# Kernel optimization log

Hardware: AMD Instinct MI355X
Metric: run time of the kernel (lower is better)

Reference implementation:

```python
import jax, jax.numpy as jnp
import numpy as np
from jax import lax

BOOST_STRENGTH = 0.5
WEIGHT_DENSITY = 0.05


def setup_inputs() -> dict:
    key = jax.random.key(0)
    k1, k2, k3, k4, k5 = jax.random.split(key, 5)
    batch, d_in, d_out = 16384, 512, 4096
    x = jax.random.normal(k1, (batch, d_in), dtype=jnp.float32)
    W = jax.random.normal(k2, (d_out, d_in), dtype=jnp.float32) * 0.05
    b = jax.random.normal(k3, (d_out,), dtype=jnp.float32) * 0.01
    w_mask = (jax.random.uniform(k4, (d_out, d_in)) < WEIGHT_DENSITY).astype(jnp.float32)
    # duty cycle buffer in [0, 0.1]
    duty_cycle = jax.random.uniform(k5, (d_out,), dtype=jnp.float32) * 0.1
    k = 205  # round(0.05 * 4096)
    return {"x": x, "W": W, "b": b, "w_mask": w_mask,
            "duty_cycle": duty_cycle, "k": k}


def reference(x, W, b, w_mask, duty_cycle, k):
    # SparseWeights: masked dense linear
    y = x @ (W * w_mask).T + b                      # [B, n]
    n = y.shape[-1]
    target_density = k / n
    # KWinners boosting: exp of duty-cycle deficit
    boost = jnp.exp(BOOST_STRENGTH * (target_density - duty_cycle))  # [n]
    boosted = y * boost                              # [B, n]
    # top-k threshold per row on boosted values
    thresh = lax.top_k(boosted, k)[0][..., -1:]      # [B, 1]
    # mask: keep ORIGINAL activations at winner positions
    return jnp.where(boosted >= thresh, y, 0.0)
```

## Files before the change

kernel.cpp:

```cpp
#include <hip/hip_runtime.h>
#include <stdint.h>
#include <math.h>


#define BATCH 16384
#define K_DIM 512
#define N_DIM 4096
#define MAXE 64
#define ROWS_A 64

typedef float f32x4 __attribute__((ext_vector_type(4)));
typedef unsigned int u32;

__global__ void boost_kernel(const float* __restrict__ duty,
                             const int* __restrict__ kptr,
                             float* __restrict__ boost) {
  const int j = blockIdx.x * blockDim.x + threadIdx.x;
  if (j < N_DIM) {
    const float td = (float)((double)kptr[0] / (double)N_DIM);
    const float arg = 0.5f * (td - duty[j]);
    boost[j] = (float)exp((double)arg);
  }
}

__global__ __launch_bounds__(256) void compress_kernel(
    const float* __restrict__ W, const float* __restrict__ mask,
    unsigned short* __restrict__ cIdx, float* __restrict__ cVal,
    int* __restrict__ cnt) {
  const int j = blockIdx.x * 4 + (threadIdx.x >> 6);
  const int lane = threadIdx.x & 63;
  if (j >= N_DIM) return;
  const float* mr = mask + (size_t)j * K_DIM;
  const float* wr = W + (size_t)j * K_DIM;
  int base = 0;
#pragma unroll
  for (int c = 0; c < K_DIM / 64; ++c) {
    const int k = c * 64 + lane;
    const bool act = (mr[k] != 0.0f);
    const unsigned long long bal = __ballot(act);
    const int pos = __popcll(bal & ((1ull << lane) - 1ull));
    if (act && base + pos < MAXE) {
      cIdx[(size_t)j * MAXE + base + pos] = (unsigned short)k;
      cVal[(size_t)j * MAXE + base + pos] = wr[k];
    }
    base += (int)__popcll(bal);
  }
  if (lane == 0) cnt[j] = base < MAXE ? base : MAXE;
}

__global__ __launch_bounds__(256) void cmax_kernel(
    const int* __restrict__ cnt, int* __restrict__ cm4) {
  const int i = blockIdx.x * 256 + threadIdx.x;
  const int4 c = *(const int4*)(cnt + i * 4);
  int m = c.x > c.y ? c.x : c.y;
  m = c.z > m ? c.z : m;
  m = c.w > m ? c.w : m;
  cm4[i] = (m + 3) & ~3;
}

__global__ __launch_bounds__(256) void fillA_kernel(
    const unsigned short* __restrict__ cIdx, const float* __restrict__ cVal,
    const int* __restrict__ cnt, uint2* __restrict__ pairsA) {
  const int idx = blockIdx.x * 256 + threadIdx.x;
  const int j = idx >> 6;
  const int e = idx & 63;
  uint2 pr;
  if (e < cnt[j]) {
    pr.x = (u32)cIdx[(size_t)j * MAXE + e] << 16;
    pr.y = __float_as_uint(cVal[(size_t)j * MAXE + e]);
  } else {
    pr.x = 0u; pr.y = 0u;
  }
  pairsA[idx] = pr;
}

__global__ __launch_bounds__(256) void transpose_kernel(
    const float* __restrict__ x, float* __restrict__ xTg) {
  __shared__ float t[64][65];
  const int lane = threadIdx.x & 63;
  const int quad = threadIdx.x >> 6;
  const int kb = (blockIdx.x & 7) * 64;
  const int rb = (blockIdx.x >> 3) * 64;
#pragma unroll
  for (int i = 0; i < 16; ++i) {
    const int r = quad * 16 + i;
    t[lane][r] = x[(size_t)(rb + r) * K_DIM + kb + lane];
  }
  __syncthreads();
#pragma unroll
  for (int i = 0; i < 16; ++i) {
    const int kq = quad * 16 + i;
    xTg[(size_t)(kb + kq) * BATCH + rb + lane] = t[kq][lane];
  }
}

__global__ __launch_bounds__(1024, 4) void fold_kernel(
    const float* __restrict__ xTg, const uint2* __restrict__ pairsA,
    const int* __restrict__ cm4, float* __restrict__ y) {
  const int tid = threadIdx.x;
  const int lane = tid & 63;
  const int wave = __builtin_amdgcn_readfirstlane(tid >> 6);
  const int row0 = blockIdx.x * ROWS_A;
  const char* xb = (const char*)(xTg + row0);
  const u32 vb = (u32)(lane << 2);

  const int jbase = wave * 256;

#pragma unroll 1
  for (int g = 0; g < 8; ++g) {
    float acc[32];
#pragma unroll
    for (int q = 0; q < 32; ++q) acc[q] = 0.0f;

#pragma unroll
    for (int sub = 0; sub < 8; ++sub) {
      const int j0 = jbase + g * 32 + sub * 4;
      const int cmax = cm4[j0 >> 2];
      const uint2* p0 = pairsA + (size_t)(j0 + 0) * MAXE;
      const uint2* p1 = pairsA + (size_t)(j0 + 1) * MAXE;
      const uint2* p2 = pairsA + (size_t)(j0 + 2) * MAXE;
      const uint2* p3 = pairsA + (size_t)(j0 + 3) * MAXE;
      float a0 = 0.0f, a1 = 0.0f, a2 = 0.0f, a3 = 0.0f;
#pragma unroll 1
      for (int e = 0; e < cmax; e += 4) {
#pragma unroll
        for (int q = 0; q < 4; ++q) {
          const uint2 e0 = p0[e + q];
          const uint2 e1 = p1[e + q];
          const uint2 e2 = p2[e + q];
          const uint2 e3 = p3[e + q];
          const float x0 = *(const float*)(xb + (e0.x + vb));
          const float x1 = *(const float*)(xb + (e1.x + vb));
          const float x2 = *(const float*)(xb + (e2.x + vb));
          const float x3 = *(const float*)(xb + (e3.x + vb));
          a0 = fmaf(__uint_as_float(e0.y), x0, a0);
          a1 = fmaf(__uint_as_float(e1.y), x1, a1);
          a2 = fmaf(__uint_as_float(e2.y), x2, a2);
          a3 = fmaf(__uint_as_float(e3.y), x3, a3);
        }
      }
      acc[sub * 4 + 0] = a0;
      acc[sub * 4 + 1] = a1;
      acc[sub * 4 + 2] = a2;
      acc[sub * 4 + 3] = a3;
    }

    float* yp = y + (size_t)(row0 + lane) * N_DIM + jbase + g * 32;
#pragma unroll
    for (int q = 0; q < 8; ++q)
      *(f32x4*)(yp + q * 4) =
          (f32x4){acc[q * 4], acc[q * 4 + 1], acc[q * 4 + 2], acc[q * 4 + 3]};
  }
}

__global__ __launch_bounds__(256) void select_kernel(
    const float* __restrict__ bvec, const float* __restrict__ boost,
    const int* __restrict__ kptr, float* __restrict__ out) {
  const int lane = threadIdx.x & 63;
  const int row = blockIdx.x * 4 + (threadIdx.x >> 6);
  const u32 kk = (u32)kptr[0];
  float* orow = out + (size_t)row * N_DIM;

  u32 kv[64];
#pragma unroll
  for (int v = 0; v < 16; ++v) {
    const int j = v * 256 + lane * 4;
    const f32x4 a = *(const f32x4*)(orow + j);
    const f32x4 b = *(const f32x4*)(bvec + j);
    const f32x4 gv = *(const f32x4*)(boost + j);
#pragma unroll
    for (int q = 0; q < 4; ++q) {
      const float yy = a[q] + b[q];
      const u32 u = __float_as_uint(yy * gv[q]);
      kv[v * 4 + q] = (u & 0x80000000u) ? ~u : (u | 0x80000000u);
    }
  }

  u32 P = 0u;
#pragma unroll 1
  for (int bit = 31; bit >= 0; --bit) {
    const u32 C = P | (1u << bit);
    u32 c0 = 0u, c1 = 0u, c2 = 0u, c3 = 0u;
#pragma unroll
    for (int s = 0; s < 16; ++s) {
      c0 += (u32)__popcll(__ballot(kv[s] >= C));
      c1 += (u32)__popcll(__ballot(kv[s + 16] >= C));
      c2 += (u32)__popcll(__ballot(kv[s + 32] >= C));
      c3 += (u32)__popcll(__ballot(kv[s + 48] >= C));
    }
    const u32 cc = (c0 + c1) + (c2 + c3);
    if (cc >= kk) P = C;
  }

#pragma unroll
  for (int v = 0; v < 16; ++v) {
    const int j = v * 256 + lane * 4;
    const f32x4 a = *(const f32x4*)(orow + j);
    const f32x4 b = *(const f32x4*)(bvec + j);
    const f32x4 gv = *(const f32x4*)(boost + j);
    f32x4 o;
#pragma unroll
    for (int q = 0; q < 4; ++q) {
      const float yy = a[q] + b[q];
      const u32 u = __float_as_uint(yy * gv[q]);
      const u32 key = (u & 0x80000000u) ? ~u : (u | 0x80000000u);
      o[q] = (key >= P) ? yy : 0.0f;
    }
    *(f32x4*)(orow + j) = o;
  }
}

extern "C" void kernel_launch(void* const* d_in, const int* in_sizes, int n_in,
                              void* d_out, int out_size, void* d_ws, size_t ws_size,
                              hipStream_t stream) {
  const float* x     = (const float*)d_in[0];
  const float* W     = (const float*)d_in[1];
  const float* bvec  = (const float*)d_in[2];
  const float* wmask = (const float*)d_in[3];
  const float* duty  = (const float*)d_in[4];
  const int* kptr    = (const int*)d_in[5];
  float* out = (float*)d_out;

  uint8_t* ws = (uint8_t*)d_ws;
  unsigned short* cIdx = (unsigned short*)(ws);
  float* cVal          = (float*)(ws + (1u << 20));
  int* cnt             = (int*)(ws + (2u << 20));
  float* boost         = (float*)(ws + (2u << 20) + (64u << 10));
  int* cm4             = (int*)(ws + (2u << 20) + (128u << 10));
  uint2* pairsA        = (uint2*)(ws + (4u << 20));
  float* xTg           = (float*)(ws + (8u << 20));

  boost_kernel<<<16, 256, 0, stream>>>(duty, kptr, boost);
  compress_kernel<<<N_DIM / 4, 256, 0, stream>>>(W, wmask, cIdx, cVal, cnt);
  cmax_kernel<<<4, 256, 0, stream>>>(cnt, cm4);
  fillA_kernel<<<(N_DIM * MAXE) / 256, 256, 0, stream>>>(cIdx, cVal, cnt, pairsA);
  transpose_kernel<<<2048, 256, 0, stream>>>(x, xTg);
  fold_kernel<<<BATCH / ROWS_A, 1024, 0, stream>>>(xTg, pairsA, cm4, out);
  select_kernel<<<BATCH / 4, 256, 0, stream>>>(bvec, boost, kptr, out);
}
```

Baseline: 887.5 us.

## Pad transposed x stride and split top-k select into threshold and apply kernels

Pads the row stride of the transposed x buffer from 16384 to 16448 floats so the gathers in the fold kernel no longer fall on power-of-two strides, which should cut cache set and channel conflicts. The lane offset moves into the base pointer, and the pair index now stores a byte offset scaled by the padded stride. The select kernel is split into a threshold-only kernel that writes one per-row threshold and a separate grid-stride apply kernel that masks the output. The split adds a second full read and write of the output along with an extra launch.

```diff
diff --git a/kernel.cpp b/kernel.cpp
--- a/kernel.cpp
+++ b/kernel.cpp
@@ -8,6 +8,7 @@
 #define N_DIM 4096
 #define MAXE 64
 #define ROWS_A 64
+#define XSTR 16448
 
 typedef float f32x4 __attribute__((ext_vector_type(4)));
 typedef unsigned int u32;
@@ -66,7 +67,7 @@
   const int e = idx & 63;
   uint2 pr;
   if (e < cnt[j]) {
-    pr.x = (u32)cIdx[(size_t)j * MAXE + e] << 16;
+    pr.x = (u32)cIdx[(size_t)j * MAXE + e] * (u32)(XSTR * 4);
     pr.y = __float_as_uint(cVal[(size_t)j * MAXE + e]);
   } else {
     pr.x = 0u; pr.y = 0u;
@@ -90,7 +91,7 @@
 #pragma unroll
   for (int i = 0; i < 16; ++i) {
     const int kq = quad * 16 + i;
-    xTg[(size_t)(kb + kq) * BATCH + rb + lane] = t[kq][lane];
+    xTg[(size_t)(kb + kq) * XSTR + rb + lane] = t[kq][lane];
   }
 }
 
@@ -101,8 +102,7 @@
   const int lane = tid & 63;
   const int wave = __builtin_amdgcn_readfirstlane(tid >> 6);
   const int row0 = blockIdx.x * ROWS_A;
-  const char* xb = (const char*)(xTg + row0);
-  const u32 vb = (u32)(lane << 2);
+  const char* xb = (const char*)(xTg + row0) + (lane << 2);
 
   const int jbase = wave * 256;
 
@@ -129,10 +129,10 @@
           const uint2 e1 = p1[e + q];
           const uint2 e2 = p2[e + q];
           const uint2 e3 = p3[e + q];
-          const float x0 = *(const float*)(xb + (e0.x + vb));
-          const float x1 = *(const float*)(xb + (e1.x + vb));
-          const float x2 = *(const float*)(xb + (e2.x + vb));
-          const float x3 = *(const float*)(xb + (e3.x + vb));
+          const float x0 = *(const float*)(xb + e0.x);
+          const float x1 = *(const float*)(xb + e1.x);
+          const float x2 = *(const float*)(xb + e2.x);
+          const float x3 = *(const float*)(xb + e3.x);
           a0 = fmaf(__uint_as_float(e0.y), x0, a0);
           a1 = fmaf(__uint_as_float(e1.y), x1, a1);
           a2 = fmaf(__uint_as_float(e2.y), x2, a2);
@@ -153,13 +153,14 @@
   }
 }
 
-__global__ __launch_bounds__(256) void select_kernel(
+__global__ __launch_bounds__(256) void thresh_kernel(
     const float* __restrict__ bvec, const float* __restrict__ boost,
-    const int* __restrict__ kptr, float* __restrict__ out) {
+    const int* __restrict__ kptr, const float* __restrict__ out,
+    u32* __restrict__ thr) {
   const int lane = threadIdx.x & 63;
   const int row = blockIdx.x * 4 + (threadIdx.x >> 6);
   const u32 kk = (u32)kptr[0];
-  float* orow = out + (size_t)row * N_DIM;
+  const float* orow = out + (size_t)row * N_DIM;
 
   u32 kv[64];
 #pragma unroll
@@ -191,13 +192,22 @@
     const u32 cc = (c0 + c1) + (c2 + c3);
     if (cc >= kk) P = C;
   }
-
-#pragma unroll
-  for (int v = 0; v < 16; ++v) {
-    const int j = v * 256 + lane * 4;
-    const f32x4 a = *(const f32x4*)(orow + j);
-    const f32x4 b = *(const f32x4*)(bvec + j);
-    const f32x4 gv = *(const f32x4*)(boost + j);
+  if (lane == 0) thr[row] = P;
+}
+
+__global__ __launch_bounds__(256) void apply_kernel(
+    const float* __restrict__ bvec, const float* __restrict__ boost,
+    const u32* __restrict__ thr, float* __restrict__ out) {
+  const int nvec = (BATCH * N_DIM) / 4;
+  const int stride = gridDim.x * 256;
+#pragma unroll 1
+  for (int idx = blockIdx.x * 256 + threadIdx.x; idx < nvec; idx += stride) {
+    const int row = idx >> 10;
+    const int c4 = (idx & 1023) * 4;
+    const u32 P = thr[row];
+    const f32x4 a = *(const f32x4*)(out + (size_t)idx * 4);
+    const f32x4 b = *(const f32x4*)(bvec + c4);
+    const f32x4 gv = *(const f32x4*)(boost + c4);
     f32x4 o;
 #pragma unroll
     for (int q = 0; q < 4; ++q) {
@@ -206,7 +216,7 @@
       const u32 key = (u & 0x80000000u) ? ~u : (u | 0x80000000u);
       o[q] = (key >= P) ? yy : 0.0f;
     }
-    *(f32x4*)(orow + j) = o;
+    *(f32x4*)(out + (size_t)idx * 4) = o;
   }
 }
 
@@ -227,8 +237,9 @@
   int* cnt             = (int*)(ws + (2u << 20));
   float* boost         = (float*)(ws + (2u << 20) + (64u << 10));
   int* cm4             = (int*)(ws + (2u << 20) + (128u << 10));
+  u32* thr             = (u32*)(ws + (2u << 20) + (192u << 10));
   uint2* pairsA        = (uint2*)(ws + (4u << 20));
-  float* xTg           = (float*)(ws + (8u << 20));
+  float* xTg           = (float*)(ws + 6815744u);
 
   boost_kernel<<<16, 256, 0, stream>>>(duty, kptr, boost);
   compress_kernel<<<N_DIM / 4, 256, 0, stream>>>(W, wmask, cIdx, cVal, cnt);
@@ -236,5 +247,6 @@
   fillA_kernel<<<(N_DIM * MAXE) / 256, 256, 0, stream>>>(cIdx, cVal, cnt, pairsA);
   transpose_kernel<<<2048, 256, 0, stream>>>(x, xTg);
   fold_kernel<<<BATCH / ROWS_A, 1024, 0, stream>>>(xTg, pairsA, cm4, out);
-  select_kernel<<<BATCH / 4, 256, 0, stream>>>(bvec, boost, kptr, out);
-}
+  thresh_kernel<<<BATCH / 4, 256, 0, stream>>>(bvec, boost, kptr, out, thr);
+  apply_kernel<<<4096, 256, 0, stream>>>(bvec, boost, thr, out);
+}
```

Result: slower. 940.8 us (+6.0%).
